# Optimization experiments

Measured on AMD Instinct MI355X. Metric: run time of the kernel, lower is better.

Reference implementation:

```python
import jax, jax.numpy as jnp
import numpy as np

L_ITERS = 8   # number of ReduNet layers
C = 10        # number of classes
D = 1024      # feature dimension
N = 4096      # number of samples (columns of Z)


def setup_inputs() -> dict:
    key = jax.random.key(0)
    k0, k1, k2, k3 = jax.random.split(key, 4)
    Z = jax.random.normal(k0, (D, N), dtype=jnp.float32)
    # column-normalized features, as the net maintains at every layer
    Z = Z / jnp.linalg.norm(Z, axis=0, keepdims=True)
    # Elist[l]: (D,D) expansion operator; Cslist[l]: (C,D,D) per-class compression operators
    Elist = jax.random.normal(k1, (L_ITERS, D, D), dtype=jnp.float32) / np.float32(np.sqrt(D))
    Cslist = jax.random.normal(k2, (L_ITERS, C, D, D), dtype=jnp.float32) / np.float32(np.sqrt(D))
    gamma = jax.random.uniform(k3, (C,), dtype=jnp.float32)
    gamma = gamma / jnp.sum(gamma)
    eta = jnp.asarray(0.5, dtype=jnp.float32)
    temperature = jnp.asarray(0.1, dtype=jnp.float32)
    return {"Z": Z, "Elist": Elist, "Cslist": Cslist, "gamma": gamma,
            "eta": eta, "temperature": temperature, "L": L_ITERS}


def reference(Z, Elist, Cslist, gamma, eta, temperature, L):
    for l in range(L):
        Cs = Cslist[l]                                   # (C, d, d)
        CZ = jnp.einsum('cij,jn->cin', Cs, Z)            # (C, d, n)
        sims = -jnp.sqrt(jnp.sum(CZ * CZ, axis=1))       # fro norm over dim=1 -> (C, n)
        P_hat = jax.nn.softmax(sims / temperature, axis=0)  # softmax over classes
        PZ = P_hat[:, None, :] * Z                       # (C, d, n)
        term = jnp.einsum('c,cij,cjn->in', gamma, Cs, PZ)   # gamma-weighted class compression
        grads = Elist[l] @ Z - term                      # (d, n)
        Z = Z + eta * grads
        Z = Z / jnp.linalg.norm(Z, axis=0, keepdims=True)   # column-wise normalization
    return Z
```

## Files before the change

### kernel.cpp

```cpp
#include <hip/hip_runtime.h>
#include <hip/hip_bf16.h>
#include <stdint.h>

#define D_DIM 1024
#define N_DIM 4096
#define C_CLS 10
#define L_IT 8
#define M_DIM 11264
#define NBM 44

typedef __bf16 bf16_t;
typedef __bf16 bf16x8 __attribute__((ext_vector_type(8)));
typedef __bf16 bf16x4 __attribute__((ext_vector_type(4)));
typedef float  f32x4  __attribute__((ext_vector_type(4)));
typedef unsigned short u16x8 __attribute__((ext_vector_type(8)));

__device__ __forceinline__ float bf2f(uint16_t u) {
  union { uint32_t i; float f; } x; x.i = ((uint32_t)u) << 16; return x.f;
}

__global__ void pack_bf16_k(const float4* __restrict__ src, bf16x4* __restrict__ dst, int n4) {
  int stride = gridDim.x * blockDim.x;
  for (int i = blockIdx.x * blockDim.x + threadIdx.x; i < n4; i += stride) {
    float4 v = src[i];
    bf16x4 o;
    o[0] = (bf16_t)v.x; o[1] = (bf16_t)v.y; o[2] = (bf16_t)v.z; o[3] = (bf16_t)v.w;
    dst[i] = o;
  }
}

__global__ __launch_bounds__(256) void init_zt(const float* __restrict__ Zin,
                                               float* __restrict__ ZfT,
                                               bf16_t* __restrict__ ZbT) {
  __shared__ float tile[32][33];
  int tx = threadIdx.x & 31, ty = threadIdx.x >> 5;
  int nb = blockIdx.x, db = blockIdx.y;
  int n = nb * 32 + tx;
#pragma unroll
  for (int j = 0; j < 32; j += 8) {
    int d = db * 32 + ty + j;
    tile[ty + j][tx] = Zin[(size_t)d * N_DIM + n];
  }
  __syncthreads();
  int d2 = db * 32 + tx;
#pragma unroll
  for (int j = 0; j < 32; j += 8) {
    int n2 = nb * 32 + ty + j;
    float v = tile[tx][ty + j];
    ZfT[(size_t)n2 * D_DIM + d2] = v;
    ZbT[(size_t)n2 * D_DIM + d2] = (bf16_t)v;
  }
}

__global__ __launch_bounds__(256) void final_out(const float* __restrict__ ZfT,
                                                 float* __restrict__ outp) {
  __shared__ float tile[32][33];
  int tx = threadIdx.x & 31, ty = threadIdx.x >> 5;
  int nb = blockIdx.x, db = blockIdx.y;
#pragma unroll
  for (int j = 0; j < 32; j += 8) {
    int n = nb * 32 + ty + j;
    int d = db * 32 + tx;
    tile[ty + j][tx] = ZfT[(size_t)n * D_DIM + d];
  }
  __syncthreads();
#pragma unroll
  for (int j = 0; j < 32; j += 8) {
    int d2 = db * 32 + ty + j;
    int n2 = nb * 32 + tx;
    outp[(size_t)d2 * N_DIM + n2] = tile[tx][ty + j];
  }
}


#define STAGE_A(buf, h, t) do {                                                         \
    _Pragma("unroll") for (int e_ = 0; e_ < 2; ++e_) {                                  \
      const bf16_t* s_ = Wb + aoff0[e_] + (size_t)(h) * 65536 + (size_t)(t) * 64;       \
      __builtin_amdgcn_global_load_lds(                                                 \
        (const __attribute__((address_space(1))) void*)s_,                              \
        (__attribute__((address_space(3))) void*)(lds + (buf)*16384 + (h)*8192 + dstslot[e_]), \
        16, 0, 0);                                                                      \
    } } while (0)

#define STAGE_B(buf, h, t) do {                                                         \
    _Pragma("unroll") for (int e_ = 0; e_ < 2; ++e_) {                                  \
      const bf16_t* s_ = ZbT + boff0[e_] + (size_t)(h) * 32768 + (size_t)(t) * 64;      \
      __builtin_amdgcn_global_load_lds(                                                 \
        (const __attribute__((address_space(1))) void*)s_,                              \
        (__attribute__((address_space(3))) void*)(lds + 32768 + (buf)*16384 + (h)*8192 + dstslot[e_]), \
        16, 0, 0);                                                                      \
    } } while (0)

#define LOAD_A(buf, qm) do {                                                            \
    _Pragma("unroll") for (int f_ = 0; f_ < 4; ++f_)                                    \
      _Pragma("unroll") for (int kk_ = 0; kk_ < 2; ++kk_)                               \
        a[f_][kk_] = *(const bf16x8*)(lds + (buf)*16384 + (qm)*8192 + aRowBase + f_*1024 + sidx[kk_]); \
  } while (0)

#define LOAD_B(buf, qn) do {                                                            \
    _Pragma("unroll") for (int f_ = 0; f_ < 2; ++f_)                                    \
      _Pragma("unroll") for (int kk_ = 0; kk_ < 2; ++kk_)                               \
        b[f_][kk_] = *(const bf16x8*)(lds + 32768 + (buf)*16384 + (qn)*8192 + bRowBase + f_*1024 + sidx[kk_]); \
  } while (0)

#define MFMA_Q(qm, qn) do {                                                             \
    _Pragma("unroll") for (int mm_ = 0; mm_ < 4; ++mm_)                                 \
      _Pragma("unroll") for (int nn_ = 0; nn_ < 2; ++nn_)                               \
        _Pragma("unroll") for (int kk_ = 0; kk_ < 2; ++kk_)                             \
          acc[(qm)*4+mm_][(qn)*2+nn_] = __builtin_amdgcn_mfma_f32_16x16x32_bf16(        \
            a[mm_][kk_], b[nn_][kk_], acc[(qm)*4+mm_][(qn)*2+nn_], 0, 0, 0);            \
  } while (0)

#define PHASE(buf, qm, qn, DO_LOADA, STAGE_STMT, WAIT_STMT) do {                        \
    if (DO_LOADA) LOAD_A(buf, qm);                                                      \
    LOAD_B(buf, qn);                                                                    \
    STAGE_STMT;                                                                         \
    __builtin_amdgcn_s_barrier();                                                       \
    asm volatile("s_waitcnt lgkmcnt(0)" ::: "memory");                                  \
    __builtin_amdgcn_sched_barrier(0);                                                  \
    __builtin_amdgcn_s_setprio(1);                                                      \
    MFMA_Q(qm, qn);                                                                     \
    __builtin_amdgcn_s_setprio(0);                                                      \
    WAIT_STMT;                                                                          \
    __builtin_amdgcn_s_barrier();                                                       \
  } while (0)

__global__ __launch_bounds__(512, 2) void gemm_wz8(const bf16_t* __restrict__ Wb,
                                                   const bf16_t* __restrict__ ZbT,
                                                   bf16_t* __restrict__ OUT_T, int ldn,
                                                   float* __restrict__ ssq) {
  __shared__ __align__(16) bf16_t lds[65536];

  int nwg = gridDim.x;
  int bid = blockIdx.x;
  int q = nwg >> 3, r = nwg & 7;
  int xcd = bid & 7, idx = bid >> 3;
  int swz = (xcd < r ? xcd * (q + 1) : r * (q + 1) + (xcd - r) * q) + idx;
  int bm = swz % NBM, bn = swz / NBM;
  int m0 = bm * 256, n0 = bn * 256;

  int tid = threadIdx.x;
  int wave = tid >> 6, lane = tid & 63;
  int wrow = wave >> 2, wcol = wave & 3;
  int lm = lane & 15, lks = lane >> 4;
  int sw = lm & 7;

  size_t aoff0[2], boff0[2];
  int dstslot[2];
#pragma unroll
  for (int e = 0; e < 2; ++e) {
    int j = e * 512 + tid;
    int rih = j >> 3, sl = j & 7;
    int sg = sl ^ (rih & 7);
    int arow = (rih & 63) + ((rih >> 6) << 7);
    int brow = (rih & 31) + ((rih >> 5) << 6);
    aoff0[e] = (size_t)(m0 + arow) * 1024 + sg * 8;
    boff0[e] = (size_t)(n0 + brow) * 1024 + sg * 8;
    dstslot[e] = e * 4096 + wave * 512;
  }

  int aRowBase = (wrow * 64 + lm) * 64;
  int bRowBase = (wcol * 32 + lm) * 64;
  int sidx[2] = { ((0 + lks) ^ sw) * 8, ((4 + lks) ^ sw) * 8 };

  f32x4 acc[8][4] = {};
  bf16x8 a[4][2], b[2][2];

  STAGE_A(0, 0, 0); STAGE_A(0, 1, 0); STAGE_B(0, 0, 0); STAGE_B(0, 1, 0);
  STAGE_A(1, 0, 1); STAGE_B(1, 0, 1);
  asm volatile("s_waitcnt vmcnt(4)" ::: "memory");
  __builtin_amdgcn_s_barrier();

  for (int it = 0; it < 7; ++it) {
    int tO = 2 * it + 1, tN = 2 * it + 2, tM = 2 * it + 3;
    PHASE(0, 0, 0, 1, STAGE_A(1, 1, tO), );
    PHASE(0, 0, 1, 0, STAGE_B(1, 1, tO), );
    PHASE(0, 1, 0, 1, STAGE_A(0, 0, tN), );
    PHASE(0, 1, 1, 0, STAGE_A(0, 1, tN), asm volatile("s_waitcnt vmcnt(4)" ::: "memory"));
    PHASE(1, 0, 0, 1, STAGE_B(0, 0, tN), );
    PHASE(1, 0, 1, 0, STAGE_B(0, 1, tN), );
    PHASE(1, 1, 0, 1, STAGE_A(1, 0, tM), );
    PHASE(1, 1, 1, 0, STAGE_B(1, 0, tM), asm volatile("s_waitcnt vmcnt(4)" ::: "memory"));
  }
  PHASE(0, 0, 0, 1, STAGE_A(1, 1, 15), );
  PHASE(0, 0, 1, 0, STAGE_B(1, 1, 15), );
  PHASE(0, 1, 0, 1, , );
  PHASE(0, 1, 1, 0, , asm volatile("s_waitcnt vmcnt(0)" ::: "memory"));
  PHASE(1, 0, 0, 1, , );
  PHASE(1, 0, 1, 0, , );
  PHASE(1, 1, 0, 1, , );
  PHASE(1, 1, 1, 0, , );

#pragma unroll
  for (int mf = 0; mf < 8; ++mf)
#pragma unroll
    for (int nf = 0; nf < 4; ++nf) {
      int col = n0 + wcol * 64 + nf * 16 + lm;
      int row = m0 + wrow * 128 + mf * 16 + lks * 4;
      bf16x4 v;
#pragma unroll
      for (int rr = 0; rr < 4; ++rr) v[rr] = (bf16_t)acc[mf][nf][rr];
      *(bf16x4*)(OUT_T + (size_t)col * M_DIM + row) = v;
    }

  if (m0 < C_CLS * 1024) {
    int c = m0 >> 10;
#pragma unroll
    for (int nf = 0; nf < 4; ++nf) {
      float v = 0.f;
#pragma unroll
      for (int mf = 0; mf < 8; ++mf)
#pragma unroll
        for (int rr = 0; rr < 4; ++rr)
          v += acc[mf][nf][rr] * acc[mf][nf][rr];
      v += __shfl_xor(v, 16);
      v += __shfl_xor(v, 32);
      if (lks == 0)
        atomicAdd(&ssq[(size_t)c * ldn + n0 + wcol * 64 + nf * 16 + lm], v);
    }
  }
}

__global__ __launch_bounds__(256) void update2(const bf16_t* __restrict__ OUT_T, int Nc,
                                               const float* __restrict__ ssq,
                                               const float* __restrict__ gamma,
                                               const float* __restrict__ etap,
                                               const float* __restrict__ tempr,
                                               float* __restrict__ ZfT,
                                               bf16_t* __restrict__ ZbT,
                                               int n_off) {
  int wv = threadIdx.x >> 6, lane = threadIdx.x & 63;
  int nl = blockIdx.x * 4 + wv;
  if (nl >= Nc) return;
  int n = n_off + nl;
  float eta = etap[0], invT = 1.0f / tempr[0];

  float s[C_CLS], m = -1e30f;
#pragma unroll
  for (int c = 0; c < C_CLS; ++c) {
    float sim = -sqrtf(ssq[(size_t)c * Nc + nl]);
    s[c] = sim;
    m = fmaxf(m, sim);
  }
  float sum = 0.f;
#pragma unroll
  for (int c = 0; c < C_CLS; ++c) {
    float e = __expf((s[c] - m) * invT);
    s[c] = e;
    sum += e;
  }
  float invsum = 1.0f / sum;
  float gP[C_CLS];
#pragma unroll
  for (int c = 0; c < C_CLS; ++c) gP[c] = gamma[c] * s[c] * invsum;

  const u16x8* ob = (const u16x8*)(OUT_T + (size_t)nl * M_DIM) + lane * 2;
  float term[16] = {};
#pragma unroll
  for (int c = 0; c < C_CLS; ++c) {
    u16x8 v0 = ob[c * 128], v1 = ob[c * 128 + 1];
#pragma unroll
    for (int j = 0; j < 8; ++j) {
      term[j]     += gP[c] * bf2f(v0[j]);
      term[8 + j] += gP[c] * bf2f(v1[j]);
    }
  }
  u16x8 g0 = ob[C_CLS * 128], g1 = ob[C_CLS * 128 + 1];

  const f32x4* zp = (const f32x4*)(ZfT + (size_t)n * D_DIM) + lane * 4;
  f32x4 z[4] = { zp[0], zp[1], zp[2], zp[3] };

  float zn[16];
  float ss = 0.f;
#pragma unroll
  for (int j = 0; j < 16; ++j) {
    float g = bf2f(j < 8 ? g0[j & 7] : g1[j & 7]);
    float v = z[j >> 2][j & 3] + eta * (g - term[j]);
    zn[j] = v;
    ss += v * v;
  }
#pragma unroll
  for (int k = 1; k < 64; k <<= 1) ss += __shfl_xor(ss, k);
  float inv = rsqrtf(ss);

  f32x4* zo = (f32x4*)(ZfT + (size_t)n * D_DIM) + lane * 4;
  bf16x8* bo = (bf16x8*)(ZbT + (size_t)n * D_DIM) + lane * 2;
#pragma unroll
  for (int q4 = 0; q4 < 4; ++q4) {
    f32x4 o;
#pragma unroll
    for (int j = 0; j < 4; ++j) o[j] = zn[q4 * 4 + j] * inv;
    zo[q4] = o;
  }
#pragma unroll
  for (int h = 0; h < 2; ++h) {
    bf16x8 o;
#pragma unroll
    for (int j = 0; j < 8; ++j) o[j] = (bf16_t)(zn[h * 8 + j] * inv);
    bo[h] = o;
  }
}

extern "C" void kernel_launch(void* const* d_in, const int* in_sizes, int n_in,
                              void* d_out, int out_size, void* d_ws, size_t ws_size,
                              hipStream_t stream) {
  (void)in_sizes; (void)n_in; (void)out_size;
  const float* Zin        = (const float*)d_in[0];
  const float* Elist      = (const float*)d_in[1];
  const float* Cslist     = (const float*)d_in[2];
  const float* gamma      = (const float*)d_in[3];
  const float* eta        = (const float*)d_in[4];
  const float* temperature= (const float*)d_in[5];

  auto align256 = [](size_t x) { return (x + 255) & ~(size_t)255; };
  size_t zbt_b = align256((size_t)N_DIM * D_DIM * 2);
  size_t zft_b = align256((size_t)N_DIM * D_DIM * 4);
  size_t wb_b  = align256((size_t)M_DIM * D_DIM * 2);
  size_t fixed = zbt_b + zft_b + wb_b;

  int Nc = N_DIM;
  while (Nc > 256) {
    size_t need = fixed + align256((size_t)C_CLS * Nc * 4) + align256((size_t)M_DIM * Nc * 2);
    if (need <= ws_size) break;
    Nc >>= 1;
  }
  if (fixed + align256((size_t)C_CLS * Nc * 4) + align256((size_t)M_DIM * Nc * 2) > ws_size) {
    hipMemsetAsync(d_out, 0, (size_t)D_DIM * N_DIM * 4, stream);
    return;
  }

  char* p = (char*)d_ws;
  bf16_t* ZbT  = (bf16_t*)p; p += zbt_b;
  float*  ZfT  = (float*)p;  p += zft_b;
  bf16_t* Wb   = (bf16_t*)p; p += wb_b;
  float*  ssq  = (float*)p;  p += align256((size_t)C_CLS * Nc * 4);
  bf16_t* OUT_T= (bf16_t*)p;

  init_zt<<<dim3(N_DIM / 32, D_DIM / 32), 256, 0, stream>>>(Zin, ZfT, ZbT);

  for (int l = 0; l < L_IT; ++l) {
    const float* Cs = Cslist + (size_t)l * C_CLS * D_DIM * D_DIM;
    const float* El = Elist  + (size_t)l * D_DIM * D_DIM;
    pack_bf16_k<<<2048, 256, 0, stream>>>((const float4*)Cs, (bf16x4*)Wb,
                                          C_CLS * D_DIM * D_DIM / 4);
    pack_bf16_k<<<1024, 256, 0, stream>>>((const float4*)El,
                                          (bf16x4*)(Wb + (size_t)C_CLS * D_DIM * D_DIM),
                                          D_DIM * D_DIM / 4);

    for (int n_off = 0; n_off < N_DIM; n_off += Nc) {
      hipMemsetAsync(ssq, 0, (size_t)C_CLS * Nc * 4, stream);
      gemm_wz8<<<dim3(NBM * (Nc / 256)), 512, 0, stream>>>(
          Wb, ZbT + (size_t)n_off * D_DIM, OUT_T, Nc, ssq);
      update2<<<dim3(Nc / 4), 256, 0, stream>>>(
          OUT_T, Nc, ssq, gamma, eta, temperature, ZfT, ZbT, n_off);
    }
  }
  final_out<<<dim3(N_DIM / 32, D_DIM / 32), 256, 0, stream>>>(ZfT, (float*)d_out);
}
```

Before: 1.278 ms.

## Fuse weight packing, hoist ssq memset, reuse B fragments across A quadrants

Merges the two bf16 pack kernels into one launch and replaces the per-layer ssq memsets with a single upfront memset over a per-layer ssq buffer. It also drops the N-chunking fallback, so the workspace must now hold the full problem or the output is zeroed. Inside the GEMM, B fragments are loaded once into two register sets (b0/b1) and reused across both A quadrants, cutting LDS reads at the cost of extra VGPRs. The aim is fewer launches and less LDS traffic.

```diff
diff --git a/kernel.cpp b/kernel.cpp
--- a/kernel.cpp
+++ b/kernel.cpp
@@ -19,14 +19,15 @@
   union { uint32_t i; float f; } x; x.i = ((uint32_t)u) << 16; return x.f;
 }
 
-__global__ void pack_bf16_k(const float4* __restrict__ src, bf16x4* __restrict__ dst, int n4) {
-  int stride = gridDim.x * blockDim.x;
-  for (int i = blockIdx.x * blockDim.x + threadIdx.x; i < n4; i += stride) {
-    float4 v = src[i];
-    bf16x4 o;
-    o[0] = (bf16_t)v.x; o[1] = (bf16_t)v.y; o[2] = (bf16_t)v.z; o[3] = (bf16_t)v.w;
-    dst[i] = o;
-  }
+__global__ __launch_bounds__(256) void pack_w(const float4* __restrict__ Cs,
+                                              const float4* __restrict__ El,
+                                              bf16x4* __restrict__ dst) {
+  const int CS4 = C_CLS * D_DIM * D_DIM / 4;
+  int i = blockIdx.x * 256 + threadIdx.x;
+  float4 v = (i < CS4) ? Cs[i] : El[i - CS4];
+  bf16x4 o;
+  o[0] = (bf16_t)v.x; o[1] = (bf16_t)v.y; o[2] = (bf16_t)v.z; o[3] = (bf16_t)v.w;
+  dst[i] = o;
 }
 
 __global__ __launch_bounds__(256) void init_zt(const float* __restrict__ Zin,
@@ -97,29 +98,28 @@
         a[f_][kk_] = *(const bf16x8*)(lds + (buf)*16384 + (qm)*8192 + aRowBase + f_*1024 + sidx[kk_]); \
   } while (0)
 
-#define LOAD_B(buf, qn) do {                                                            \
+#define LOAD_Bq(buf, qn, arr) do {                                                      \
     _Pragma("unroll") for (int f_ = 0; f_ < 2; ++f_)                                    \
       _Pragma("unroll") for (int kk_ = 0; kk_ < 2; ++kk_)                               \
-        b[f_][kk_] = *(const bf16x8*)(lds + 32768 + (buf)*16384 + (qn)*8192 + bRowBase + f_*1024 + sidx[kk_]); \
+        arr[f_][kk_] = *(const bf16x8*)(lds + 32768 + (buf)*16384 + (qn)*8192 + bRowBase + f_*1024 + sidx[kk_]); \
   } while (0)
 
-#define MFMA_Q(qm, qn) do {                                                             \
+#define MFMA_Q(qm, qn, arr) do {                                                        \
     _Pragma("unroll") for (int mm_ = 0; mm_ < 4; ++mm_)                                 \
       _Pragma("unroll") for (int nn_ = 0; nn_ < 2; ++nn_)                               \
         _Pragma("unroll") for (int kk_ = 0; kk_ < 2; ++kk_)                             \
           acc[(qm)*4+mm_][(qn)*2+nn_] = __builtin_amdgcn_mfma_f32_16x16x32_bf16(        \
-            a[mm_][kk_], b[nn_][kk_], acc[(qm)*4+mm_][(qn)*2+nn_], 0, 0, 0);            \
+            a[mm_][kk_], arr[nn_][kk_], acc[(qm)*4+mm_][(qn)*2+nn_], 0, 0, 0);          \
   } while (0)
 
-#define PHASE(buf, qm, qn, DO_LOADA, STAGE_STMT, WAIT_STMT) do {                        \
-    if (DO_LOADA) LOAD_A(buf, qm);                                                      \
-    LOAD_B(buf, qn);                                                                    \
+#define PHASE(qm, qn, arr, LOAD_STMT, STAGE_STMT, WAIT_STMT) do {                       \
+    LOAD_STMT;                                                                          \
     STAGE_STMT;                                                                         \
     __builtin_amdgcn_s_barrier();                                                       \
     asm volatile("s_waitcnt lgkmcnt(0)" ::: "memory");                                  \
     __builtin_amdgcn_sched_barrier(0);                                                  \
     __builtin_amdgcn_s_setprio(1);                                                      \
-    MFMA_Q(qm, qn);                                                                     \
+    MFMA_Q(qm, qn, arr);                                                                \
     __builtin_amdgcn_s_setprio(0);                                                      \
     WAIT_STMT;                                                                          \
     __builtin_amdgcn_s_barrier();                                                       \
@@ -164,7 +164,7 @@
   int sidx[2] = { ((0 + lks) ^ sw) * 8, ((4 + lks) ^ sw) * 8 };
 
   f32x4 acc[8][4] = {};
-  bf16x8 a[4][2], b[2][2];
+  bf16x8 a[4][2], b0[2][2], b1[2][2];
 
   STAGE_A(0, 0, 0); STAGE_A(0, 1, 0); STAGE_B(0, 0, 0); STAGE_B(0, 1, 0);
   STAGE_A(1, 0, 1); STAGE_B(1, 0, 1);
@@ -173,23 +173,23 @@
 
   for (int it = 0; it < 7; ++it) {
     int tO = 2 * it + 1, tN = 2 * it + 2, tM = 2 * it + 3;
-    PHASE(0, 0, 0, 1, STAGE_A(1, 1, tO), );
-    PHASE(0, 0, 1, 0, STAGE_B(1, 1, tO), );
-    PHASE(0, 1, 0, 1, STAGE_A(0, 0, tN), );
-    PHASE(0, 1, 1, 0, STAGE_A(0, 1, tN), asm volatile("s_waitcnt vmcnt(4)" ::: "memory"));
-    PHASE(1, 0, 0, 1, STAGE_B(0, 0, tN), );
-    PHASE(1, 0, 1, 0, STAGE_B(0, 1, tN), );
-    PHASE(1, 1, 0, 1, STAGE_A(1, 0, tM), );
-    PHASE(1, 1, 1, 0, STAGE_B(1, 0, tM), asm volatile("s_waitcnt vmcnt(4)" ::: "memory"));
-  }
-  PHASE(0, 0, 0, 1, STAGE_A(1, 1, 15), );
-  PHASE(0, 0, 1, 0, STAGE_B(1, 1, 15), );
-  PHASE(0, 1, 0, 1, , );
-  PHASE(0, 1, 1, 0, , asm volatile("s_waitcnt vmcnt(0)" ::: "memory"));
-  PHASE(1, 0, 0, 1, , );
-  PHASE(1, 0, 1, 0, , );
-  PHASE(1, 1, 0, 1, , );
-  PHASE(1, 1, 1, 0, , );
+    PHASE(0, 0, b0, LOAD_A(0,0); LOAD_Bq(0,0,b0), STAGE_A(1, 1, tO), );
+    PHASE(0, 1, b1, LOAD_Bq(0,1,b1),              STAGE_B(1, 1, tO), );
+    PHASE(1, 0, b0, LOAD_A(0,1),                  STAGE_A(0, 0, tN), );
+    PHASE(1, 1, b1, ,                             STAGE_A(0, 1, tN), asm volatile("s_waitcnt vmcnt(4)" ::: "memory"));
+    PHASE(0, 0, b0, LOAD_A(1,0); LOAD_Bq(1,0,b0), STAGE_B(0, 0, tN), );
+    PHASE(0, 1, b1, LOAD_Bq(1,1,b1),              STAGE_B(0, 1, tN), );
+    PHASE(1, 0, b0, LOAD_A(1,1),                  STAGE_A(1, 0, tM), );
+    PHASE(1, 1, b1, ,                             STAGE_B(1, 0, tM), asm volatile("s_waitcnt vmcnt(4)" ::: "memory"));
+  }
+  PHASE(0, 0, b0, LOAD_A(0,0); LOAD_Bq(0,0,b0), STAGE_A(1, 1, 15), );
+  PHASE(0, 1, b1, LOAD_Bq(0,1,b1),              STAGE_B(1, 1, 15), );
+  PHASE(1, 0, b0, LOAD_A(0,1),                  , );
+  PHASE(1, 1, b1, ,                             , asm volatile("s_waitcnt vmcnt(0)" ::: "memory"));
+  PHASE(0, 0, b0, LOAD_A(1,0); LOAD_Bq(1,0,b0), , );
+  PHASE(0, 1, b1, LOAD_Bq(1,1,b1),              , );
+  PHASE(1, 0, b0, LOAD_A(1,1),                  , );
+  PHASE(1, 1, b1, ,                             , );
 
 #pragma unroll
   for (int mf = 0; mf < 8; ++mf)
@@ -316,15 +316,10 @@
   size_t zbt_b = align256((size_t)N_DIM * D_DIM * 2);
   size_t zft_b = align256((size_t)N_DIM * D_DIM * 4);
   size_t wb_b  = align256((size_t)M_DIM * D_DIM * 2);
-  size_t fixed = zbt_b + zft_b + wb_b;
-
-  int Nc = N_DIM;
-  while (Nc > 256) {
-    size_t need = fixed + align256((size_t)C_CLS * Nc * 4) + align256((size_t)M_DIM * Nc * 2);
-    if (need <= ws_size) break;
-    Nc >>= 1;
-  }
-  if (fixed + align256((size_t)C_CLS * Nc * 4) + align256((size_t)M_DIM * Nc * 2) > ws_size) {
+  size_t ssq_b = align256((size_t)L_IT * C_CLS * N_DIM * 4);
+  size_t out_b = align256((size_t)M_DIM * N_DIM * 2);
+
+  if (zbt_b + zft_b + wb_b + ssq_b + out_b > ws_size) {
     hipMemsetAsync(d_out, 0, (size_t)D_DIM * N_DIM * 4, stream);
     return;
   }
@@ -333,27 +328,24 @@
   bf16_t* ZbT  = (bf16_t*)p; p += zbt_b;
   float*  ZfT  = (float*)p;  p += zft_b;
   bf16_t* Wb   = (bf16_t*)p; p += wb_b;
-  float*  ssq  = (float*)p;  p += align256((size_t)C_CLS * Nc * 4);
+  float*  ssq  = (float*)p;  p += ssq_b;
   bf16_t* OUT_T= (bf16_t*)p;
 
+  hipMemsetAsync(ssq, 0, (size_t)L_IT * C_CLS * N_DIM * 4, stream);
   init_zt<<<dim3(N_DIM / 32, D_DIM / 32), 256, 0, stream>>>(Zin, ZfT, ZbT);
 
   for (int l = 0; l < L_IT; ++l) {
     const float* Cs = Cslist + (size_t)l * C_CLS * D_DIM * D_DIM;
     const float* El = Elist  + (size_t)l * D_DIM * D_DIM;
-    pack_bf16_k<<<2048, 256, 0, stream>>>((const float4*)Cs, (bf16x4*)Wb,
-                                          C_CLS * D_DIM * D_DIM / 4);
-    pack_bf16_k<<<1024, 256, 0, stream>>>((const float4*)El,
-                                          (bf16x4*)(Wb + (size_t)C_CLS * D_DIM * D_DIM),
-                                          D_DIM * D_DIM / 4);
-
-    for (int n_off = 0; n_off < N_DIM; n_off += Nc) {
-      hipMemsetAsync(ssq, 0, (size_t)C_CLS * Nc * 4, stream);
-      gemm_wz8<<<dim3(NBM * (Nc / 256)), 512, 0, stream>>>(
-          Wb, ZbT + (size_t)n_off * D_DIM, OUT_T, Nc, ssq);
-      update2<<<dim3(Nc / 4), 256, 0, stream>>>(
-          OUT_T, Nc, ssq, gamma, eta, temperature, ZfT, ZbT, n_off);
-    }
+    float* ssq_l = ssq + (size_t)l * C_CLS * N_DIM;
+
+    pack_w<<<dim3(M_DIM * D_DIM / 4 / 256), 256, 0, stream>>>(
+        (const float4*)Cs, (const float4*)El, (bf16x4*)Wb);
+
+    gemm_wz8<<<dim3(NBM * (N_DIM / 256)), 512, 0, stream>>>(
+        Wb, ZbT, OUT_T, N_DIM, ssq_l);
+    update2<<<dim3(N_DIM / 4), 256, 0, stream>>>(
+        OUT_T, N_DIM, ssq_l, gamma, eta, temperature, ZfT, ZbT, 0);
   }
   final_out<<<dim3(N_DIM / 32, D_DIM / 32), 256, 0, stream>>>(ZfT, (float*)d_out);
 }
```

After: 1.244 ms. 2.6% less time.
